# Kernel tuning notes

Hardware: AMD Instinct MI355X
Metric: run time of the kernel (lower is better)

## Reference

```python
import jax, jax.numpy as jnp
import numpy as np

N = 2048       # num nodes
E = 4096       # num edges
D_NODE = 128
D_EDGE = 128
H = 4          # heads
DH = D_EDGE // H
C = 16         # num classes
NODE_K = N // 2   # node_k_ratio = 0.5
EDGE_K = E // 2   # edge_k_ratio = 0.5
NEG = -1e9


def setup_inputs() -> dict:
    key = jax.random.key(0)
    ks = jax.random.split(key, 16)
    w = lambda k, shape: jax.random.normal(k, shape, jnp.float32) * 0.02
    return {
        "node_features": jax.random.normal(ks[0], (N, D_NODE), jnp.float32),
        "edge_features": jax.random.normal(ks[1], (E, D_EDGE), jnp.float32),
        "edge_index": jax.random.randint(ks[2], (2, E), 0, N, jnp.int32),
        # ImportanceRouter: scalar scores per node / edge
        "w_router_n": w(ks[3], (D_NODE,)),
        "w_router_e": w(ks[4], (D_EDGE,)),
        # EdgeAttention projections
        "w_e": w(ks[5], (D_EDGE, D_EDGE)),
        "w_n": w(ks[6], (D_NODE, D_EDGE)),
        "w_q": w(ks[7], (D_EDGE, D_EDGE)),
        "w_k": w(ks[8], (D_EDGE, D_EDGE)),
        "w_v": w(ks[9], (D_EDGE, D_EDGE)),
        "w_o": w(ks[10], (D_EDGE, D_EDGE)),
        # classifier MLP: Linear -> GELU -> Linear
        "w1": w(ks[11], (D_EDGE, D_EDGE)),
        "b1": jnp.zeros((D_EDGE,), jnp.float32),
        "w2": w(ks[12], (D_EDGE, C)),
        "b2": jnp.zeros((C,), jnp.float32),
    }


def reference(node_features, edge_features, edge_index,
              w_router_n, w_router_e,
              w_e, w_n, w_q, w_k, w_v, w_o,
              w1, b1, w2, b2):
    src, dst = edge_index[0], edge_index[1]

    # --- ImportanceRouter: node/edge scores ---
    ns = node_features @ w_router_n   # [N]
    es = edge_features @ w_router_e   # [E]

    # --- apply_top_k(node_k_ratio=0.5, edge_k_ratio=0.5) ---
    _, nidx = jax.lax.top_k(ns, NODE_K)
    node_mask = jnp.zeros((N,), bool).at[nidx].set(True)
    _, eidx = jax.lax.top_k(es, EDGE_K)
    edge_topk = jnp.zeros((E,), bool).at[eidx].set(True)
    edge_mask = edge_topk & node_mask[src] & node_mask[dst]   # [E]

    ef = edge_features * edge_mask[:, None].astype(edge_features.dtype)

    # --- build_edge_adjacency: edges sharing a node attend to each other ---
    adj = ((src[:, None] == src[None, :]) | (src[:, None] == dst[None, :]) |
           (dst[:, None] == src[None, :]) | (dst[:, None] == dst[None, :]))  # [E,E]

    # --- EdgeAttention: edge rep mixes edge feats and endpoint node feats ---
    h = ef @ w_e + (node_features[src] + node_features[dst]) @ w_n   # [E, D_EDGE]
    q = (h @ w_q).reshape(E, H, DH)
    k = (h @ w_k).reshape(E, H, DH)
    v = (h @ w_v).reshape(E, H, DH)
    scores = jnp.einsum('ehd,fhd->hef', q, k) / np.float32(np.sqrt(DH))  # [H,E,E]
    scores = jnp.where(adj[None, :, :], scores, NEG)
    attn = jax.nn.softmax(scores, axis=-1)
    o = jnp.einsum('hef,fhd->ehd', attn, v).reshape(E, D_EDGE) @ w_o    # [E, D_EDGE]

    # --- classifier: Linear -> GELU -> Linear ---
    x = jax.nn.gelu(o @ w1 + b1)
    logits = x @ w2 + b2            # [E, C]
    return logits
```

## Files before the change

kernel.cpp:

```cpp
#include <hip/hip_runtime.h>
#include <hip/hip_bf16.h>
#include <math.h>

#define NN 2048
#define NE 4096
#define D 128
#define NODE_K 1024
#define EDGE_K 2048
#define CAP 64

typedef const __hip_bfloat16* bfp;
typedef __attribute__((ext_vector_type(8))) short short8;
typedef __attribute__((ext_vector_type(4))) float floatx4;

#define MFMA16(a, b, c) __builtin_amdgcn_mfma_f32_16x16x32_bf16(a, b, c, 0, 0, 0)

__device__ __forceinline__ float b2f(__hip_bfloat16 x) { return __bfloat162float(x); }

__device__ __forceinline__ float ldx(const void* p, size_t i, int f) {
  return f ? ((const float*)p)[i] : b2f(((bfp)p)[i]);
}
__device__ __forceinline__ float4 ldx4(const void* p, size_t i4, int f) {
  if (f) return ((const float4*)p)[i4];
  ushort4 u = ((const ushort4*)p)[i4];
  float4 r;
  r.x = __uint_as_float(((unsigned)u.x) << 16);
  r.y = __uint_as_float(((unsigned)u.y) << 16);
  r.z = __uint_as_float(((unsigned)u.z) << 16);
  r.w = __uint_as_float(((unsigned)u.w) << 16);
  return r;
}

__device__ __forceinline__ void split2(float x, unsigned short& hi, unsigned short& lo) {
  unsigned u = __float_as_uint(x);
  unsigned h = (u + 0x7FFFu + ((u >> 16) & 1u)) >> 16;
  hi = (unsigned short)h;
  float r = x - __uint_as_float(h << 16);
  unsigned v = __float_as_uint(r);
  lo = (unsigned short)((v + 0x7FFFu + ((v >> 16) & 1u)) >> 16);
}
__device__ __forceinline__ void build_frags(const float* v8, short8& fh, short8& fl) {
  #pragma unroll
  for (int i = 0; i < 8; ++i) {
    unsigned short h, l;
    split2(v8[i], h, l);
    fh[i] = (short)h; fl[i] = (short)l;
  }
}

__device__ __forceinline__ int detect_f(const unsigned short* raw, int* s4) {
  int t = threadIdx.x;
  int weird = 0;
  for (int i = t; i < 4096; i += blockDim.x) {
    unsigned int bits = ((unsigned int)raw[i]) << 16;
    float x = __uint_as_float(bits);
    float ax = fabsf(x);
    if (!(ax <= 1e3f) || (x != 0.f && ax < 1e-12f)) weird++;
  }
  #pragma unroll
  for (int m = 32; m >= 1; m >>= 1) weird += __shfl_xor(weird, m);
  int nw = (int)blockDim.x >> 6;
  if ((t & 63) == 0) s4[t >> 6] = weird;
  __syncthreads();
  int tot = 0;
  for (int i = 0; i < nw; ++i) tot += s4[i];
  return (tot > 200) ? 1 : 0;
}

struct K1Args {
  const void *nf, *ef, *wrn, *wre;
  const void* w[7];
  float *ns, *es;
  int *deg, *flag;
  unsigned short *wtHi, *wtLo;
};

#define SCORE_BLOCKS ((NN + NE) / 4)
#define WPREP_BLOCKS 56
__global__ __launch_bounds__(256) void scores_prep_kernel(K1Args a) {
  __shared__ int s4[4];
  int b = blockIdx.x, t = threadIdx.x;
  int f = detect_f((const unsigned short*)a.nf, s4);
  if (b < SCORE_BLOCKS) {
    int wid = b * 4 + (t >> 6), lane = t & 63;
    const void* base; const void* w; float* out; size_t r0;
    if (wid < NN) { base = a.nf; r0 = (size_t)wid * D; w = a.wrn; out = a.ns + wid; }
    else { int r = wid - NN; base = a.ef; r0 = (size_t)r * D; w = a.wre; out = a.es + r; }
    double p = (double)ldx(base, r0 + lane, f) * (double)ldx(w, lane, f)
             + (double)ldx(base, r0 + lane + 64, f) * (double)ldx(w, lane + 64, f);
    #pragma unroll
    for (int m = 32; m >= 1; m >>= 1) p += __shfl_xor(p, m);
    if (lane == 0) *out = (float)p;
  } else if (b == SCORE_BLOCKS) {
    if (t == 0) a.flag[0] = f;
    for (int i = t; i < NN; i += 256) a.deg[i] = 0;
  } else {
    int wb = b - SCORE_BLOCKS - 1;
    #pragma unroll
    for (int i = 0; i < 8; ++i) {
      int g = wb * 2048 + i * 256 + t;
      int w = g >> 14, r = g & 16383;
      int k = r >> 7, n = r & 127;
      float x = ldx(a.w[w], r, f);
      unsigned short hi, lo;
      split2(x, hi, lo);
      a.wtHi[w * 16384 + n * 128 + k] = hi;
      a.wtLo[w * 16384 + n * 128 + k] = lo;
    }
  }
}

#define NMB (NN / 4)
#define EMB (NE / 4)
__global__ __launch_bounds__(256) void mask_lists_kernel(
    const float* __restrict__ ns, const float* __restrict__ es,
    const int* __restrict__ src, const int* __restrict__ dst,
    int* __restrict__ node_mask, int* __restrict__ edge_topk,
    int* __restrict__ deg, int* __restrict__ lists) {
  __shared__ float s[NE];
  int b = blockIdx.x, t = threadIdx.x;
  if (b < NMB) {
    for (int i = t; i < NN; i += 256) s[i] = ns[i];
    __syncthreads();
    int i = b * 4 + (t >> 6), lane = t & 63;
    float si = s[i];
    int rank = 0;
    for (int j = lane; j < NN; j += 64) {
      float sj = s[j];
      rank += (sj > si) || (sj == si && j < i);
    }
    #pragma unroll
    for (int m = 32; m >= 1; m >>= 1) rank += __shfl_xor(rank, m);
    if (lane == 0) node_mask[i] = (rank < NODE_K) ? 1 : 0;
  } else if (b < NMB + EMB) {
    for (int i = t; i < NE; i += 256) s[i] = es[i];
    __syncthreads();
    int i = (b - NMB) * 4 + (t >> 6), lane = t & 63;
    float si = s[i];
    int rank = 0;
    for (int j = lane; j < NE; j += 64) {
      float sj = s[j];
      rank += (sj > si) || (sj == si && j < i);
    }
    #pragma unroll
    for (int m = 32; m >= 1; m >>= 1) rank += __shfl_xor(rank, m);
    if (lane == 0) edge_topk[i] = (rank < EDGE_K) ? 1 : 0;
  } else {
    int e = (b - NMB - EMB) * 256 + t;
    if (e < NE) {
      int sn = src[e], dn = dst[e];
      int p = atomicAdd(&deg[sn], 1);
      if (p >= 0 && p < CAP) lists[sn * CAP + p] = e;
      if (dn != sn) {
        p = atomicAdd(&deg[dn], 1);
        if (p >= 0 && p < CAP) lists[dn * CAP + p] = e;
      }
    }
  }
}

__global__ __launch_bounds__(512) void h_qkv_mfma_kernel(
    const void* __restrict__ ef, const void* __restrict__ nf,
    const int* __restrict__ src, const int* __restrict__ dst,
    const int* __restrict__ node_mask, const int* __restrict__ edge_topk,
    const int* __restrict__ flag,
    const unsigned short* __restrict__ wtHi, const unsigned short* __restrict__ wtLo,
    float* __restrict__ qkv) {
  __shared__ __align__(16) float hf[8 * 64 * 4];
  int t = threadIdx.x;
  int wave = t >> 6, lane = t & 63;
  int q = lane >> 4, c = lane & 15;
  int f = flag[0];
  int row0 = blockIdx.x * 16;
  int e = row0 + c;
  int sn = src[e], dn = dst[e];
  float em = (edge_topk[e] && node_mask[sn] && node_mask[dn]) ? 1.f : 0.f;
  int n0 = wave * 16;
  const unsigned short* WEh = wtHi;             const unsigned short* WEl = wtLo;
  const unsigned short* WNh = wtHi + 16384;     const unsigned short* WNl = wtLo + 16384;

  floatx4 acc = {0.f, 0.f, 0.f, 0.f};
  #pragma unroll
  for (int ks = 0; ks < 4; ++ks) {
    int k0 = ks * 32 + q * 8;
    size_t i4 = ((size_t)e * D + k0) >> 2;
    float4 e0 = ldx4(ef, i4, f), e1 = ldx4(ef, i4 + 1, f);
    size_t s4i = ((size_t)sn * D + k0) >> 2;
    size_t d4i = ((size_t)dn * D + k0) >> 2;
    float4 s0 = ldx4(nf, s4i, f), s1 = ldx4(nf, s4i + 1, f);
    float4 d0 = ldx4(nf, d4i, f), d1 = ldx4(nf, d4i + 1, f);
    float a1[8] = {em * e0.x, em * e0.y, em * e0.z, em * e0.w,
                   em * e1.x, em * e1.y, em * e1.z, em * e1.w};
    float a2[8] = {s0.x + d0.x, s0.y + d0.y, s0.z + d0.z, s0.w + d0.w,
                   s1.x + d1.x, s1.y + d1.y, s1.z + d1.z, s1.w + d1.w};
    short8 a1h, a1l, a2h, a2l;
    build_frags(a1, a1h, a1l);
    build_frags(a2, a2h, a2l);
    size_t bo = (size_t)(n0 + c) * 128 + k0;
    short8 bEh = *(const short8*)(WEh + bo);
    short8 bEl = *(const short8*)(WEl + bo);
    short8 bNh = *(const short8*)(WNh + bo);
    short8 bNl = *(const short8*)(WNl + bo);
    acc = MFMA16(a1h, bEh, acc);
    acc = MFMA16(a1l, bEh, acc);
    acc = MFMA16(a1h, bEl, acc);
    acc = MFMA16(a2h, bNh, acc);
    acc = MFMA16(a2l, bNh, acc);
    acc = MFMA16(a2h, bNl, acc);
  }
  {
    int np = n0 + c;
    int kd = np >> 5, qd = (np >> 3) & 3, half = (c >> 2) & 1, j4 = c & 3;
    #pragma unroll
    for (int r = 0; r < 4; ++r) {
      int destlane = qd * 16 + 4 * q + r;
      hf[((kd * 2 + half) * 64 + destlane) * 4 + j4] = acc[r];
    }
  }
  __syncthreads();
  #pragma unroll
  for (int sel = 0; sel < 3; ++sel) {
    const unsigned short* Bh = wtHi + (size_t)(2 + sel) * 16384;
    const unsigned short* Bl = wtLo + (size_t)(2 + sel) * 16384;
    floatx4 a2c = {0.f, 0.f, 0.f, 0.f};
    #pragma unroll
    for (int ks = 0; ks < 4; ++ks) {
      float4 p0 = *(const float4*)&hf[((ks * 2 + 0) * 64 + lane) * 4];
      float4 p1 = *(const float4*)&hf[((ks * 2 + 1) * 64 + lane) * 4];
      float v8[8] = {p0.x, p0.y, p0.z, p0.w, p1.x, p1.y, p1.z, p1.w};
      short8 ah, al;
      build_frags(v8, ah, al);
      size_t bo = (size_t)(n0 + c) * 128 + ks * 32 + q * 8;
      short8 bh = *(const short8*)(Bh + bo);
      short8 bl = *(const short8*)(Bl + bo);
      a2c = MFMA16(ah, bh, a2c);
      a2c = MFMA16(al, bh, a2c);
      a2c = MFMA16(ah, bl, a2c);
    }
    float* C = qkv + (size_t)sel * NE * D;
    #pragma unroll
    for (int r = 0; r < 4; ++r)
      C[(size_t)(row0 + 4 * q + r) * D + n0 + c] = a2c[r];
  }
}

__global__ void attn_kernel(const float* __restrict__ q, const float* __restrict__ k,
                            const float* __restrict__ v, const int* __restrict__ src,
                            const int* __restrict__ dst, const int* __restrict__ deg,
                            const int* __restrict__ lists, float* __restrict__ ao) {
  int e = blockIdx.x;
  int j = threadIdx.x;
  float qj = q[e * D + j];
  int sn = src[e], dn = dst[e];
  float m = -1e30f, l = 0.f, acc = 0.f;
  const float scale = 0.17677669529663687f;
  int degA = max(0, min(deg[sn], CAP));
  for (int i = 0; i < degA; ++i) {
    int fe = lists[sn * CAP + i];
    float p = qj * k[fe * D + j];
    p += __shfl_xor(p, 16); p += __shfl_xor(p, 8); p += __shfl_xor(p, 4);
    p += __shfl_xor(p, 2);  p += __shfl_xor(p, 1);
    float s = p * scale;
    float vj = v[fe * D + j];
    float mn = fmaxf(m, s);
    float corr = expf(m - mn);
    float w = expf(s - mn);
    l = l * corr + w;
    acc = acc * corr + w * vj;
    m = mn;
  }
  if (dn != sn) {
    int degB = max(0, min(deg[dn], CAP));
    for (int i = 0; i < degB; ++i) {
      int fe = lists[dn * CAP + i];
      if (src[fe] == sn || dst[fe] == sn) continue;
      float p = qj * k[fe * D + j];
      p += __shfl_xor(p, 16); p += __shfl_xor(p, 8); p += __shfl_xor(p, 4);
      p += __shfl_xor(p, 2);  p += __shfl_xor(p, 1);
      float s = p * scale;
      float vj = v[fe * D + j];
      float mn = fmaxf(m, s);
      float corr = expf(m - mn);
      float w = expf(s - mn);
      l = l * corr + w;
      acc = acc * corr + w * vj;
      m = mn;
    }
  }
  ao[e * D + j] = acc / fmaxf(l, 1e-37f);
}

__global__ __launch_bounds__(512) void o_mlp_mfma_kernel(
    const float* __restrict__ ao,
    const unsigned short* __restrict__ wtHi, const unsigned short* __restrict__ wtLo,
    const void* __restrict__ b1, const void* __restrict__ w2,
    const void* __restrict__ b2, const int* __restrict__ flag,
    void* __restrict__ out) {
  __shared__ __align__(16) float hf[8 * 64 * 4];
  __shared__ float xl[16 * 132];
  __shared__ float w2l[128 * 16];
  int t = threadIdx.x;
  int wave = t >> 6, lane = t & 63;
  int q = lane >> 4, c = lane & 15;
  int f = flag[0];
  int row0 = blockIdx.x * 16;
  int n0 = wave * 16;
  const unsigned short* WOh = wtHi + 5 * 16384;
  const unsigned short* WOl = wtLo + 5 * 16384;
  const unsigned short* W1h = wtHi + 6 * 16384;
  const unsigned short* W1l = wtLo + 6 * 16384;

  floatx4 acc = {0.f, 0.f, 0.f, 0.f};
  #pragma unroll
  for (int ks = 0; ks < 4; ++ks) {
    int k0 = ks * 32 + q * 8;
    const float* ap = ao + (size_t)(row0 + c) * D + k0;
    float4 p0 = *(const float4*)ap;
    float4 p1 = *(const float4*)(ap + 4);
    float v8[8] = {p0.x, p0.y, p0.z, p0.w, p1.x, p1.y, p1.z, p1.w};
    short8 ah, al;
    build_frags(v8, ah, al);
    size_t bo = (size_t)(n0 + c) * 128 + k0;
    short8 bh = *(const short8*)(WOh + bo);
    short8 bl = *(const short8*)(WOl + bo);
    acc = MFMA16(ah, bh, acc);
    acc = MFMA16(al, bh, acc);
    acc = MFMA16(ah, bl, acc);
  }
  {
    int np = n0 + c;
    int kd = np >> 5, qd = (np >> 3) & 3, half = (c >> 2) & 1, j4 = c & 3;
    #pragma unroll
    for (int r = 0; r < 4; ++r)
      hf[((kd * 2 + half) * 64 + qd * 16 + 4 * q + r) * 4 + j4] = acc[r];
  }
  __syncthreads();
  floatx4 a2c = {0.f, 0.f, 0.f, 0.f};
  #pragma unroll
  for (int ks = 0; ks < 4; ++ks) {
    float4 p0 = *(const float4*)&hf[((ks * 2 + 0) * 64 + lane) * 4];
    float4 p1 = *(const float4*)&hf[((ks * 2 + 1) * 64 + lane) * 4];
    float v8[8] = {p0.x, p0.y, p0.z, p0.w, p1.x, p1.y, p1.z, p1.w};
    short8 ah, al;
    build_frags(v8, ah, al);
    size_t bo = (size_t)(n0 + c) * 128 + ks * 32 + q * 8;
    short8 bh = *(const short8*)(W1h + bo);
    short8 bl = *(const short8*)(W1l + bo);
    a2c = MFMA16(ah, bh, a2c);
    a2c = MFMA16(al, bh, a2c);
    a2c = MFMA16(ah, bl, a2c);
  }
  float bj = ldx(b1, n0 + c, f);
  #pragma unroll
  for (int r = 0; r < 4; ++r) {
    float u = a2c[r] + bj;
    float inner = 0.7978845608028654f * (u + 0.044715f * u * u * u);
    xl[(4 * q + r) * 132 + n0 + c] = 0.5f * u * (1.f + tanhf(inner));
  }
  for (int i = t; i < D * 16; i += 512) w2l[i] = ldx(w2, i, f);
  __syncthreads();
  if (t < 256) {
    int r = t >> 4, cc = t & 15;
    float s = 0.f;
    for (int kk = 0; kk < D; ++kk) s += xl[r * 132 + kk] * w2l[kk * 16 + cc];
    s += ldx(b2, cc, f);
    int idx = (row0 + r) * 16 + cc;
    if (f) ((float*)out)[idx] = s;
    else ((__hip_bfloat16*)out)[idx] = __float2bfloat16(s);
  }
}

extern "C" void kernel_launch(void* const* d_in, const int* in_sizes, int n_in,
                              void* d_out, int out_size, void* d_ws, size_t ws_size,
                              hipStream_t stream) {
  const int* eidx = (const int*)d_in[2];
  const int* src = eidx;
  const int* dst = eidx + NE;

  size_t off = 0;
  char* base = (char*)d_ws;
  auto alloc = [&](size_t nbytes) -> void* {
    void* p = base + off;
    off += (nbytes + 255) & ~(size_t)255;
    return p;
  };
  int* flag              = (int*)alloc(256);
  float* ns              = (float*)alloc(NN * sizeof(float));
  float* es              = (float*)alloc(NE * sizeof(float));
  int* node_mask         = (int*)alloc(NN * sizeof(int));
  int* edge_topk         = (int*)alloc(NE * sizeof(int));
  int* deg               = (int*)alloc(NN * sizeof(int));
  int* lists             = (int*)alloc((size_t)NN * CAP * sizeof(int));
  unsigned short* wtHi   = (unsigned short*)alloc((size_t)7 * 16384 * sizeof(unsigned short));
  unsigned short* wtLo   = (unsigned short*)alloc((size_t)7 * 16384 * sizeof(unsigned short));
  float* qkv             = (float*)alloc((size_t)3 * NE * D * sizeof(float));
  float* ao              = (float*)alloc((size_t)NE * D * sizeof(float));
  float* qb = qkv, *kb = qkv + NE * D, *vb = qkv + 2 * NE * D;

  K1Args a1;
  a1.nf = d_in[0]; a1.ef = d_in[1]; a1.wrn = d_in[3]; a1.wre = d_in[4];
  a1.w[0] = d_in[5];  a1.w[1] = d_in[6];  a1.w[2] = d_in[7];
  a1.w[3] = d_in[8];  a1.w[4] = d_in[9];  a1.w[5] = d_in[10]; a1.w[6] = d_in[11];
  a1.ns = ns; a1.es = es; a1.deg = deg; a1.flag = flag;
  a1.wtHi = wtHi; a1.wtLo = wtLo;

  scores_prep_kernel<<<SCORE_BLOCKS + 1 + WPREP_BLOCKS, 256, 0, stream>>>(a1);
  mask_lists_kernel<<<NMB + EMB + NE / 256, 256, 0, stream>>>(
      ns, es, src, dst, node_mask, edge_topk, deg, lists);
  h_qkv_mfma_kernel<<<NE / 16, 512, 0, stream>>>(
      d_in[1], d_in[0], src, dst, node_mask, edge_topk, flag, wtHi, wtLo, qkv);
  attn_kernel<<<NE, 128, 0, stream>>>(qb, kb, vb, src, dst, deg, lists, ao);
  o_mlp_mfma_kernel<<<NE / 16, 512, 0, stream>>>(
      ao, wtHi, wtLo, d_in[12], d_in[13], d_in[14], flag, d_out);
}
```

Before: 146.4 us.

## Fuse attention into output MLP kernel and presplit features to bf16 hi/lo

Merges the per-edge attention kernel with the o-projection/MLP kernel so attention outputs stay in shared memory rather than round-tripping through a global buffer, removing one launch. Node and edge features are now split into bf16 hi/lo once in the prep kernel, so the h/QKV kernel loads ready-made fragments instead of converting them per use. That kernel also computes Q, K and V in a single pass with interleaved MFMAs. In exchange, the src+dst sum is now done as separate MFMAs, which adds matrix work, and attention now runs in 512-thread blocks covering 16 edges, which changes occupancy and load balance across degree-varying edges.

```diff
diff --git a/kernel.cpp b/kernel.cpp
--- a/kernel.cpp
+++ b/kernel.cpp
@@ -10,6 +10,7 @@
 #define CAP 64
 
 typedef const __hip_bfloat16* bfp;
+typedef unsigned short u16;
 typedef __attribute__((ext_vector_type(8))) short short8;
 typedef __attribute__((ext_vector_type(4))) float floatx4;
 
@@ -20,35 +21,25 @@
 __device__ __forceinline__ float ldx(const void* p, size_t i, int f) {
   return f ? ((const float*)p)[i] : b2f(((bfp)p)[i]);
 }
-__device__ __forceinline__ float4 ldx4(const void* p, size_t i4, int f) {
-  if (f) return ((const float4*)p)[i4];
-  ushort4 u = ((const ushort4*)p)[i4];
-  float4 r;
-  r.x = __uint_as_float(((unsigned)u.x) << 16);
-  r.y = __uint_as_float(((unsigned)u.y) << 16);
-  r.z = __uint_as_float(((unsigned)u.z) << 16);
-  r.w = __uint_as_float(((unsigned)u.w) << 16);
-  return r;
-}
-
-__device__ __forceinline__ void split2(float x, unsigned short& hi, unsigned short& lo) {
+
+__device__ __forceinline__ void split2(float x, u16& hi, u16& lo) {
   unsigned u = __float_as_uint(x);
   unsigned h = (u + 0x7FFFu + ((u >> 16) & 1u)) >> 16;
-  hi = (unsigned short)h;
+  hi = (u16)h;
   float r = x - __uint_as_float(h << 16);
   unsigned v = __float_as_uint(r);
-  lo = (unsigned short)((v + 0x7FFFu + ((v >> 16) & 1u)) >> 16);
+  lo = (u16)((v + 0x7FFFu + ((v >> 16) & 1u)) >> 16);
 }
 __device__ __forceinline__ void build_frags(const float* v8, short8& fh, short8& fl) {
   #pragma unroll
   for (int i = 0; i < 8; ++i) {
-    unsigned short h, l;
+    u16 h, l;
     split2(v8[i], h, l);
     fh[i] = (short)h; fl[i] = (short)l;
   }
 }
 
-__device__ __forceinline__ int detect_f(const unsigned short* raw, int* s4) {
+__device__ __forceinline__ int detect_f(const u16* raw, int* s4) {
   int t = threadIdx.x;
   int weird = 0;
   for (int i = t; i < 4096; i += blockDim.x) {
@@ -72,15 +63,17 @@
   const void* w[7];
   float *ns, *es;
   int *deg, *flag;
-  unsigned short *wtHi, *wtLo;
+  u16 *wtHi, *wtLo;
+  u16 *feHi, *feLo;
 };
 
 #define SCORE_BLOCKS ((NN + NE) / 4)
 #define WPREP_BLOCKS 56
+#define FSPLIT_BLOCKS 384
 __global__ __launch_bounds__(256) void scores_prep_kernel(K1Args a) {
   __shared__ int s4[4];
   int b = blockIdx.x, t = threadIdx.x;
-  int f = detect_f((const unsigned short*)a.nf, s4);
+  int f = detect_f((const u16*)a.nf, s4);
   if (b < SCORE_BLOCKS) {
     int wid = b * 4 + (t >> 6), lane = t & 63;
     const void* base; const void* w; float* out; size_t r0;
@@ -94,18 +87,27 @@
   } else if (b == SCORE_BLOCKS) {
     if (t == 0) a.flag[0] = f;
     for (int i = t; i < NN; i += 256) a.deg[i] = 0;
-  } else {
+  } else if (b <= SCORE_BLOCKS + WPREP_BLOCKS) {
     int wb = b - SCORE_BLOCKS - 1;
     #pragma unroll
     for (int i = 0; i < 8; ++i) {
       int g = wb * 2048 + i * 256 + t;
       int w = g >> 14, r = g & 16383;
       int k = r >> 7, n = r & 127;
-      float x = ldx(a.w[w], r, f);
-      unsigned short hi, lo;
-      split2(x, hi, lo);
+      u16 hi, lo;
+      split2(ldx(a.w[w], r, f), hi, lo);
       a.wtHi[w * 16384 + n * 128 + k] = hi;
       a.wtLo[w * 16384 + n * 128 + k] = lo;
+    }
+  } else {
+    int fb = b - SCORE_BLOCKS - 1 - WPREP_BLOCKS;
+    #pragma unroll
+    for (int i = 0; i < 8; ++i) {
+      int g = fb * 2048 + i * 256 + t;
+      float x = (g < NN * D) ? ldx(a.nf, g, f) : ldx(a.ef, g - NN * D, f);
+      u16 hi, lo;
+      split2(x, hi, lo);
+      a.feHi[g] = hi; a.feLo[g] = lo;
     }
   }
 }
@@ -160,125 +162,122 @@
 }
 
 __global__ __launch_bounds__(512) void h_qkv_mfma_kernel(
-    const void* __restrict__ ef, const void* __restrict__ nf,
+    const u16* __restrict__ feHi, const u16* __restrict__ feLo,
     const int* __restrict__ src, const int* __restrict__ dst,
     const int* __restrict__ node_mask, const int* __restrict__ edge_topk,
-    const int* __restrict__ flag,
-    const unsigned short* __restrict__ wtHi, const unsigned short* __restrict__ wtLo,
+    const u16* __restrict__ wtHi, const u16* __restrict__ wtLo,
     float* __restrict__ qkv) {
   __shared__ __align__(16) float hf[8 * 64 * 4];
   int t = threadIdx.x;
   int wave = t >> 6, lane = t & 63;
-  int q = lane >> 4, c = lane & 15;
-  int f = flag[0];
+  int qd = lane >> 4, c = lane & 15;
   int row0 = blockIdx.x * 16;
   int e = row0 + c;
   int sn = src[e], dn = dst[e];
-  float em = (edge_topk[e] && node_mask[sn] && node_mask[dn]) ? 1.f : 0.f;
+  bool em = edge_topk[e] && node_mask[sn] && node_mask[dn];
   int n0 = wave * 16;
-  const unsigned short* WEh = wtHi;             const unsigned short* WEl = wtLo;
-  const unsigned short* WNh = wtHi + 16384;     const unsigned short* WNl = wtLo + 16384;
+  const u16* efH = feHi + (size_t)NN * D;
+  const u16* efL = feLo + (size_t)NN * D;
+  const short8 z8 = {0, 0, 0, 0, 0, 0, 0, 0};
 
   floatx4 acc = {0.f, 0.f, 0.f, 0.f};
   #pragma unroll
   for (int ks = 0; ks < 4; ++ks) {
-    int k0 = ks * 32 + q * 8;
-    size_t i4 = ((size_t)e * D + k0) >> 2;
-    float4 e0 = ldx4(ef, i4, f), e1 = ldx4(ef, i4 + 1, f);
-    size_t s4i = ((size_t)sn * D + k0) >> 2;
-    size_t d4i = ((size_t)dn * D + k0) >> 2;
-    float4 s0 = ldx4(nf, s4i, f), s1 = ldx4(nf, s4i + 1, f);
-    float4 d0 = ldx4(nf, d4i, f), d1 = ldx4(nf, d4i + 1, f);
-    float a1[8] = {em * e0.x, em * e0.y, em * e0.z, em * e0.w,
-                   em * e1.x, em * e1.y, em * e1.z, em * e1.w};
-    float a2[8] = {s0.x + d0.x, s0.y + d0.y, s0.z + d0.z, s0.w + d0.w,
-                   s1.x + d1.x, s1.y + d1.y, s1.z + d1.z, s1.w + d1.w};
-    short8 a1h, a1l, a2h, a2l;
-    build_frags(a1, a1h, a1l);
-    build_frags(a2, a2h, a2l);
+    int k0 = ks * 32 + qd * 8;
+    short8 a1h = *(const short8*)(efH + (size_t)e * D + k0);
+    short8 a1l = *(const short8*)(efL + (size_t)e * D + k0);
+    if (!em) { a1h = z8; a1l = z8; }
+    short8 sh = *(const short8*)(feHi + (size_t)sn * D + k0);
+    short8 sl = *(const short8*)(feLo + (size_t)sn * D + k0);
+    short8 dh = *(const short8*)(feHi + (size_t)dn * D + k0);
+    short8 dl = *(const short8*)(feLo + (size_t)dn * D + k0);
     size_t bo = (size_t)(n0 + c) * 128 + k0;
-    short8 bEh = *(const short8*)(WEh + bo);
-    short8 bEl = *(const short8*)(WEl + bo);
-    short8 bNh = *(const short8*)(WNh + bo);
-    short8 bNl = *(const short8*)(WNl + bo);
+    short8 bEh = *(const short8*)(wtHi + bo);
+    short8 bEl = *(const short8*)(wtLo + bo);
+    short8 bNh = *(const short8*)(wtHi + 16384 + bo);
+    short8 bNl = *(const short8*)(wtLo + 16384 + bo);
     acc = MFMA16(a1h, bEh, acc);
     acc = MFMA16(a1l, bEh, acc);
     acc = MFMA16(a1h, bEl, acc);
-    acc = MFMA16(a2h, bNh, acc);
-    acc = MFMA16(a2l, bNh, acc);
-    acc = MFMA16(a2h, bNl, acc);
+    acc = MFMA16(sh, bNh, acc);
+    acc = MFMA16(sl, bNh, acc);
+    acc = MFMA16(sh, bNl, acc);
+    acc = MFMA16(dh, bNh, acc);
+    acc = MFMA16(dl, bNh, acc);
+    acc = MFMA16(dh, bNl, acc);
   }
   {
     int np = n0 + c;
-    int kd = np >> 5, qd = (np >> 3) & 3, half = (c >> 2) & 1, j4 = c & 3;
-    #pragma unroll
-    for (int r = 0; r < 4; ++r) {
-      int destlane = qd * 16 + 4 * q + r;
-      hf[((kd * 2 + half) * 64 + destlane) * 4 + j4] = acc[r];
-    }
+    int kd = np >> 5, qq = (np >> 3) & 3, half = (c >> 2) & 1, j4 = c & 3;
+    #pragma unroll
+    for (int r = 0; r < 4; ++r)
+      hf[((kd * 2 + half) * 64 + qq * 16 + 4 * qd + r) * 4 + j4] = acc[r];
   }
   __syncthreads();
-  #pragma unroll
-  for (int sel = 0; sel < 3; ++sel) {
-    const unsigned short* Bh = wtHi + (size_t)(2 + sel) * 16384;
-    const unsigned short* Bl = wtLo + (size_t)(2 + sel) * 16384;
-    floatx4 a2c = {0.f, 0.f, 0.f, 0.f};
-    #pragma unroll
-    for (int ks = 0; ks < 4; ++ks) {
-      float4 p0 = *(const float4*)&hf[((ks * 2 + 0) * 64 + lane) * 4];
-      float4 p1 = *(const float4*)&hf[((ks * 2 + 1) * 64 + lane) * 4];
-      float v8[8] = {p0.x, p0.y, p0.z, p0.w, p1.x, p1.y, p1.z, p1.w};
-      short8 ah, al;
-      build_frags(v8, ah, al);
-      size_t bo = (size_t)(n0 + c) * 128 + ks * 32 + q * 8;
-      short8 bh = *(const short8*)(Bh + bo);
-      short8 bl = *(const short8*)(Bl + bo);
-      a2c = MFMA16(ah, bh, a2c);
-      a2c = MFMA16(al, bh, a2c);
-      a2c = MFMA16(ah, bl, a2c);
-    }
-    float* C = qkv + (size_t)sel * NE * D;
-    #pragma unroll
-    for (int r = 0; r < 4; ++r)
-      C[(size_t)(row0 + 4 * q + r) * D + n0 + c] = a2c[r];
-  }
-}
-
-__global__ void attn_kernel(const float* __restrict__ q, const float* __restrict__ k,
-                            const float* __restrict__ v, const int* __restrict__ src,
-                            const int* __restrict__ dst, const int* __restrict__ deg,
-                            const int* __restrict__ lists, float* __restrict__ ao) {
-  int e = blockIdx.x;
-  int j = threadIdx.x;
-  float qj = q[e * D + j];
-  int sn = src[e], dn = dst[e];
-  float m = -1e30f, l = 0.f, acc = 0.f;
+  floatx4 aq = {0.f, 0.f, 0.f, 0.f};
+  floatx4 ak = {0.f, 0.f, 0.f, 0.f};
+  floatx4 av = {0.f, 0.f, 0.f, 0.f};
+  #pragma unroll
+  for (int ks = 0; ks < 4; ++ks) {
+    float4 p0 = *(const float4*)&hf[((ks * 2 + 0) * 64 + lane) * 4];
+    float4 p1 = *(const float4*)&hf[((ks * 2 + 1) * 64 + lane) * 4];
+    float v8[8] = {p0.x, p0.y, p0.z, p0.w, p1.x, p1.y, p1.z, p1.w};
+    short8 ah, al;
+    build_frags(v8, ah, al);
+    size_t bo = (size_t)(n0 + c) * 128 + ks * 32 + qd * 8;
+    short8 bqh = *(const short8*)(wtHi + 2 * 16384 + bo);
+    short8 bql = *(const short8*)(wtLo + 2 * 16384 + bo);
+    short8 bkh = *(const short8*)(wtHi + 3 * 16384 + bo);
+    short8 bkl = *(const short8*)(wtLo + 3 * 16384 + bo);
+    short8 bvh = *(const short8*)(wtHi + 4 * 16384 + bo);
+    short8 bvl = *(const short8*)(wtLo + 4 * 16384 + bo);
+    aq = MFMA16(ah, bqh, aq); aq = MFMA16(al, bqh, aq); aq = MFMA16(ah, bql, aq);
+    ak = MFMA16(ah, bkh, ak); ak = MFMA16(al, bkh, ak); ak = MFMA16(ah, bkl, ak);
+    av = MFMA16(ah, bvh, av); av = MFMA16(al, bvh, av); av = MFMA16(ah, bvl, av);
+  }
+  #pragma unroll
+  for (int r = 0; r < 4; ++r) {
+    size_t ro = (size_t)(row0 + 4 * qd + r) * D + n0 + c;
+    qkv[ro] = aq[r];
+    qkv[(size_t)NE * D + ro] = ak[r];
+    qkv[(size_t)2 * NE * D + ro] = av[r];
+  }
+}
+
+__global__ __launch_bounds__(512) void attn_mlp_kernel(
+    const float* __restrict__ qkv, const int* __restrict__ src,
+    const int* __restrict__ dst, const int* __restrict__ deg,
+    const int* __restrict__ lists,
+    const u16* __restrict__ wtHi, const u16* __restrict__ wtLo,
+    const void* __restrict__ b1, const void* __restrict__ w2,
+    const void* __restrict__ b2, const int* __restrict__ flag,
+    void* __restrict__ out) {
+  __shared__ __align__(16) float aol[16 * 132];
+  __shared__ __align__(16) float hf[8 * 64 * 4];
+  __shared__ float xl[16 * 132];
+  __shared__ float w2l[128 * 16];
+  int t = threadIdx.x;
+  int row0 = blockIdx.x * 16;
+  int f = flag[0];
+  const float* qp = qkv;
+  const float* kp = qkv + (size_t)NE * D;
+  const float* vp = qkv + (size_t)2 * NE * D;
   const float scale = 0.17677669529663687f;
-  int degA = max(0, min(deg[sn], CAP));
-  for (int i = 0; i < degA; ++i) {
-    int fe = lists[sn * CAP + i];
-    float p = qj * k[fe * D + j];
-    p += __shfl_xor(p, 16); p += __shfl_xor(p, 8); p += __shfl_xor(p, 4);
-    p += __shfl_xor(p, 2);  p += __shfl_xor(p, 1);
-    float s = p * scale;
-    float vj = v[fe * D + j];
-    float mn = fmaxf(m, s);
-    float corr = expf(m - mn);
-    float w = expf(s - mn);
-    l = l * corr + w;
-    acc = acc * corr + w * vj;
-    m = mn;
-  }
-  if (dn != sn) {
-    int degB = max(0, min(deg[dn], CAP));
-    for (int i = 0; i < degB; ++i) {
-      int fe = lists[dn * CAP + i];
-      if (src[fe] == sn || dst[fe] == sn) continue;
-      float p = qj * k[fe * D + j];
+  int j = t & 127;
+  for (int it = 0; it < 4; ++it) {
+    int le = it * 4 + (t >> 7);
+    int e = row0 + le;
+    float qj = qp[(size_t)e * D + j];
+    int sn = src[e], dn = dst[e];
+    float m = -1e30f, l = 0.f, acc = 0.f;
+    int degA = max(0, min(deg[sn], CAP));
+    for (int i = 0; i < degA; ++i) {
+      int fe = lists[sn * CAP + i];
+      float p = qj * kp[(size_t)fe * D + j];
       p += __shfl_xor(p, 16); p += __shfl_xor(p, 8); p += __shfl_xor(p, 4);
       p += __shfl_xor(p, 2);  p += __shfl_xor(p, 1);
       float s = p * scale;
-      float vj = v[fe * D + j];
+      float vj = vp[(size_t)fe * D + j];
       float mn = fmaxf(m, s);
       float corr = expf(m - mn);
       float w = expf(s - mn);
@@ -286,53 +285,55 @@
       acc = acc * corr + w * vj;
       m = mn;
     }
-  }
-  ao[e * D + j] = acc / fmaxf(l, 1e-37f);
-}
-
-__global__ __launch_bounds__(512) void o_mlp_mfma_kernel(
-    const float* __restrict__ ao,
-    const unsigned short* __restrict__ wtHi, const unsigned short* __restrict__ wtLo,
-    const void* __restrict__ b1, const void* __restrict__ w2,
-    const void* __restrict__ b2, const int* __restrict__ flag,
-    void* __restrict__ out) {
-  __shared__ __align__(16) float hf[8 * 64 * 4];
-  __shared__ float xl[16 * 132];
-  __shared__ float w2l[128 * 16];
-  int t = threadIdx.x;
+    if (dn != sn) {
+      int degB = max(0, min(deg[dn], CAP));
+      for (int i = 0; i < degB; ++i) {
+        int fe = lists[dn * CAP + i];
+        if (src[fe] == sn || dst[fe] == sn) continue;
+        float p = qj * kp[(size_t)fe * D + j];
+        p += __shfl_xor(p, 16); p += __shfl_xor(p, 8); p += __shfl_xor(p, 4);
+        p += __shfl_xor(p, 2);  p += __shfl_xor(p, 1);
+        float s = p * scale;
+        float vj = vp[(size_t)fe * D + j];
+        float mn = fmaxf(m, s);
+        float corr = expf(m - mn);
+        float w = expf(s - mn);
+        l = l * corr + w;
+        acc = acc * corr + w * vj;
+        m = mn;
+      }
+    }
+    aol[le * 132 + j] = acc / fmaxf(l, 1e-37f);
+  }
+  for (int i = t; i < D * 16; i += 512) w2l[i] = ldx(w2, i, f);
+  __syncthreads();
+
   int wave = t >> 6, lane = t & 63;
-  int q = lane >> 4, c = lane & 15;
-  int f = flag[0];
-  int row0 = blockIdx.x * 16;
+  int qd = lane >> 4, c = lane & 15;
   int n0 = wave * 16;
-  const unsigned short* WOh = wtHi + 5 * 16384;
-  const unsigned short* WOl = wtLo + 5 * 16384;
-  const unsigned short* W1h = wtHi + 6 * 16384;
-  const unsigned short* W1l = wtLo + 6 * 16384;
-
   floatx4 acc = {0.f, 0.f, 0.f, 0.f};
   #pragma unroll
   for (int ks = 0; ks < 4; ++ks) {
-    int k0 = ks * 32 + q * 8;
-    const float* ap = ao + (size_t)(row0 + c) * D + k0;
+    int k0 = ks * 32 + qd * 8;
+    const float* ap = aol + c * 132 + k0;
     float4 p0 = *(const float4*)ap;
     float4 p1 = *(const float4*)(ap + 4);
     float v8[8] = {p0.x, p0.y, p0.z, p0.w, p1.x, p1.y, p1.z, p1.w};
     short8 ah, al;
     build_frags(v8, ah, al);
     size_t bo = (size_t)(n0 + c) * 128 + k0;
-    short8 bh = *(const short8*)(WOh + bo);
-    short8 bl = *(const short8*)(WOl + bo);
+    short8 bh = *(const short8*)(wtHi + 5 * 16384 + bo);
+    short8 bl = *(const short8*)(wtLo + 5 * 16384 + bo);
     acc = MFMA16(ah, bh, acc);
     acc = MFMA16(al, bh, acc);
     acc = MFMA16(ah, bl, acc);
   }
   {
     int np = n0 + c;
-    int kd = np >> 5, qd = (np >> 3) & 3, half = (c >> 2) & 1, j4 = c & 3;
+    int kd = np >> 5, qq = (np >> 3) & 3, half = (c >> 2) & 1, j4 = c & 3;
     #pragma unroll
     for (int r = 0; r < 4; ++r)
-      hf[((kd * 2 + half) * 64 + qd * 16 + 4 * q + r) * 4 + j4] = acc[r];
+      hf[((kd * 2 + half) * 64 + qq * 16 + 4 * qd + r) * 4 + j4] = acc[r];
   }
   __syncthreads();
   floatx4 a2c = {0.f, 0.f, 0.f, 0.f};
@@ -343,9 +344,9 @@
     float v8[8] = {p0.x, p0.y, p0.z, p0.w, p1.x, p1.y, p1.z, p1.w};
     short8 ah, al;
     build_frags(v8, ah, al);
-    size_t bo = (size_t)(n0 + c) * 128 + ks * 32 + q * 8;
-    short8 bh = *(const short8*)(W1h + bo);
-    short8 bl = *(const short8*)(W1l + bo);
+    size_t bo = (size_t)(n0 + c) * 128 + ks * 32 + qd * 8;
+    short8 bh = *(const short8*)(wtHi + 6 * 16384 + bo);
+    short8 bl = *(const short8*)(wtLo + 6 * 16384 + bo);
     a2c = MFMA16(ah, bh, a2c);
     a2c = MFMA16(al, bh, a2c);
     a2c = MFMA16(ah, bl, a2c);
@@ -355,9 +356,8 @@
   for (int r = 0; r < 4; ++r) {
     float u = a2c[r] + bj;
     float inner = 0.7978845608028654f * (u + 0.044715f * u * u * u);
-    xl[(4 * q + r) * 132 + n0 + c] = 0.5f * u * (1.f + tanhf(inner));
-  }
-  for (int i = t; i < D * 16; i += 512) w2l[i] = ldx(w2, i, f);
+    xl[(4 * qd + r) * 132 + n0 + c] = 0.5f * u * (1.f + tanhf(inner));
+  }
   __syncthreads();
   if (t < 256) {
     int r = t >> 4, cc = t & 15;
@@ -384,32 +384,33 @@
     off += (nbytes + 255) & ~(size_t)255;
     return p;
   };
-  int* flag              = (int*)alloc(256);
-  float* ns              = (float*)alloc(NN * sizeof(float));
-  float* es              = (float*)alloc(NE * sizeof(float));
-  int* node_mask         = (int*)alloc(NN * sizeof(int));
-  int* edge_topk         = (int*)alloc(NE * sizeof(int));
-  int* deg               = (int*)alloc(NN * sizeof(int));
-  int* lists             = (int*)alloc((size_t)NN * CAP * sizeof(int));
-  unsigned short* wtHi   = (unsigned short*)alloc((size_t)7 * 16384 * sizeof(unsigned short));
-  unsigned short* wtLo   = (unsigned short*)alloc((size_t)7 * 16384 * sizeof(unsigned short));
-  float* qkv             = (float*)alloc((size_t)3 * NE * D * sizeof(float));
-  float* ao              = (float*)alloc((size_t)NE * D * sizeof(float));
-  float* qb = qkv, *kb = qkv + NE * D, *vb = qkv + 2 * NE * D;
+  int* flag      = (int*)alloc(256);
+  float* ns      = (float*)alloc(NN * sizeof(float));
+  float* es      = (float*)alloc(NE * sizeof(float));
+  int* node_mask = (int*)alloc(NN * sizeof(int));
+  int* edge_topk = (int*)alloc(NE * sizeof(int));
+  int* deg       = (int*)alloc(NN * sizeof(int));
+  int* lists     = (int*)alloc((size_t)NN * CAP * sizeof(int));
+  u16* wtHi      = (u16*)alloc((size_t)7 * 16384 * sizeof(u16));
+  u16* wtLo      = (u16*)alloc((size_t)7 * 16384 * sizeof(u16));
+  u16* feHi      = (u16*)alloc((size_t)(NN + NE) * D * sizeof(u16));
+  u16* feLo      = (u16*)alloc((size_t)(NN + NE) * D * sizeof(u16));
+  float* qkv     = (float*)alloc((size_t)3 * NE * D * sizeof(float));
 
   K1Args a1;
   a1.nf = d_in[0]; a1.ef = d_in[1]; a1.wrn = d_in[3]; a1.wre = d_in[4];
   a1.w[0] = d_in[5];  a1.w[1] = d_in[6];  a1.w[2] = d_in[7];
   a1.w[3] = d_in[8];  a1.w[4] = d_in[9];  a1.w[5] = d_in[10]; a1.w[6] = d_in[11];
   a1.ns = ns; a1.es = es; a1.deg = deg; a1.flag = flag;
-  a1.wtHi = wtHi; a1.wtLo = wtLo;
-
-  scores_prep_kernel<<<SCORE_BLOCKS + 1 + WPREP_BLOCKS, 256, 0, stream>>>(a1);
+  a1.wtHi = wtHi; a1.wtLo = wtLo; a1.feHi = feHi; a1.feLo = feLo;
+
+  scores_prep_kernel<<<SCORE_BLOCKS + 1 + WPREP_BLOCKS + FSPLIT_BLOCKS, 256, 0,
+                       stream>>>(a1);
   mask_lists_kernel<<<NMB + EMB + NE / 256, 256, 0, stream>>>(
       ns, es, src, dst, node_mask, edge_topk, deg, lists);
   h_qkv_mfma_kernel<<<NE / 16, 512, 0, stream>>>(
-      d_in[1], d_in[0], src, dst, node_mask, edge_topk, flag, wtHi, wtLo, qkv);
-  attn_kernel<<<NE, 128, 0, stream>>>(qb, kb, vb, src, dst, deg, lists, ao);
-  o_mlp_mfma_kernel<<<NE / 16, 512, 0, stream>>>(
-      ao, wtHi, wtLo, d_in[12], d_in[13], d_in[14], flag, d_out);
-}
+      feHi, feLo, src, dst, node_mask, edge_topk, wtHi, wtLo, qkv);
+  attn_mlp_kernel<<<NE / 16, 512, 0, stream>>>(
+      qkv, src, dst, deg, lists, wtHi, wtLo, d_in[12], d_in[13], d_in[14],
+      flag, d_out);
+}
```

Measured after the change: 170.3 us. 16.3% more time.
